# Kernel tuning notes

Hardware: AMD Instinct MI355X
Metric: run time of the kernel (lower is better)

## Reference

```python
import jax, jax.numpy as jnp
import numpy as np


def setup_inputs() -> dict:
    key = jax.random.key(0)
    ks = jax.random.split(key, 7)
    B, N, D, A = 32, 128, 512, 512
    sD = 1.0 / np.sqrt(D)
    sA = 1.0 / np.sqrt(A)
    return {
        "x": jax.random.normal(ks[0], (B, N, D), dtype=jnp.float32),
        "W1": jax.random.normal(ks[1], (A, D), dtype=jnp.float32) * sD,
        "b1": jax.random.normal(ks[2], (A,), dtype=jnp.float32) * sD,
        "W2": jax.random.normal(ks[3], (A, D), dtype=jnp.float32) * sD,
        "b2": jax.random.normal(ks[4], (A,), dtype=jnp.float32) * sD,
        "Wout": jax.random.normal(ks[5], (A,), dtype=jnp.float32) * sA,
        "bout": jax.random.normal(ks[6], (1,), dtype=jnp.float32) * sA,
    }


def reference(x, W1, b1, W2, b2, Wout, bout):
    # x: (B, N, D)
    x1 = jnp.einsum('bnd,ad->bna', x, W1) + b1  # mlp1 -> (B, N, A)
    x2 = jnp.einsum('bnd,ad->bna', x, W2) + b2  # mlp2 -> (B, N, A)
    # outer broadcast add: x1.unsqueeze(1) + x2.unsqueeze(2) -> (B, N, N, A)
    s = x1[:, None, :, :] + x2[:, :, None, :]
    # include_root=False: drop ROOT row along dim 1 -> (B, N-1, N, A)
    s = s[:, 1:, :, :]
    s = jnp.tanh(s)
    # out linear A -> 1, then squeeze -> (B, N-1, N)
    return jnp.einsum('bija,a->bij', s, Wout) + bout[0]
```

## Files before the change

kernel.cpp:

```cpp
#include <hip/hip_runtime.h>
#include <hip/hip_bf16.h>

#define B_ 32
#define N_ 128
#define D_ 512
#define A_ 512
#define R_ (B_*N_)
#define OC (2*A_)
#define CEXP 2.8853900817779268f

typedef __attribute__((ext_vector_type(8))) short  frag_ab;
typedef __attribute__((ext_vector_type(4))) float  frag_cd;

__device__ inline unsigned pack2bf(float a, float b) {
    unsigned ua = __builtin_bit_cast(unsigned, a) + 0x8000u;
    unsigned ub = __builtin_bit_cast(unsigned, b) + 0x8000u;
    return __builtin_amdgcn_perm(ub, ua, 0x07060302);
}

__global__ __launch_bounds__(256) void k1_mfma(
    const float* __restrict__ X,
    const float* __restrict__ W1, const float* __restrict__ b1,
    const float* __restrict__ W2, const float* __restrict__ b2,
    float* __restrict__ Y)
{
    __shared__ unsigned short As[128*32];
    __shared__ unsigned short Bs[128*32];

    const int t    = threadIdx.x;
    const int lane = t & 63;
    const int wid  = t >> 6;
    const int wr   = wid >> 1;
    const int wc   = wid & 1;
    const int row0 = blockIdx.x * 128;
    const int col0 = blockIdx.y * 128;
    const float* Wb = (col0 < A_) ? W1 : W2;
    const float* bb = (col0 < A_) ? b1 : b2;
    const int wrow0 = col0 & (A_-1);

    const int srow = t >> 2;
    const int sk8  = (t & 3) * 8;

    frag_cd acc[4][4];
#pragma unroll
    for (int i = 0; i < 4; ++i)
#pragma unroll
        for (int j = 0; j < 4; ++j) acc[i][j] = frag_cd{0.f,0.f,0.f,0.f};

    const int fr = lane & 15;
    const int ko = (lane >> 4) * 8;

    for (int k0 = 0; k0 < D_; k0 += 32) {
        float4 xv[2][2], wv[2][2];
#pragma unroll
        for (int q = 0; q < 2; ++q) {
            const int row = q*64 + srow;
            const float* px = &X [(size_t)(row0  + row) * D_ + k0 + sk8];
            const float* pw = &Wb[(size_t)(wrow0 + row) * D_ + k0 + sk8];
            xv[q][0] = *(const float4*)px;  xv[q][1] = *(const float4*)(px+4);
            wv[q][0] = *(const float4*)pw;  wv[q][1] = *(const float4*)(pw+4);
        }
        __syncthreads();
#pragma unroll
        for (int q = 0; q < 2; ++q) {
            const int row = q*64 + srow;
            uint4 pa, pb;
            pa.x = pack2bf(xv[q][0].x, xv[q][0].y);
            pa.y = pack2bf(xv[q][0].z, xv[q][0].w);
            pa.z = pack2bf(xv[q][1].x, xv[q][1].y);
            pa.w = pack2bf(xv[q][1].z, xv[q][1].w);
            pb.x = pack2bf(wv[q][0].x, wv[q][0].y);
            pb.y = pack2bf(wv[q][0].z, wv[q][0].w);
            pb.z = pack2bf(wv[q][1].x, wv[q][1].y);
            pb.w = pack2bf(wv[q][1].z, wv[q][1].w);
            *reinterpret_cast<uint4*>(&As[row*32 + sk8]) = pa;
            *reinterpret_cast<uint4*>(&Bs[row*32 + sk8]) = pb;
        }
        __syncthreads();
        frag_ab af[4], bfv[4];
#pragma unroll
        for (int fi = 0; fi < 4; ++fi)
            af[fi]  = *reinterpret_cast<const frag_ab*>(&As[(wr*64 + fi*16 + fr)*32 + ko]);
#pragma unroll
        for (int fj = 0; fj < 4; ++fj)
            bfv[fj] = *reinterpret_cast<const frag_ab*>(&Bs[(wc*64 + fj*16 + fr)*32 + ko]);
#pragma unroll
        for (int fi = 0; fi < 4; ++fi)
#pragma unroll
            for (int fj = 0; fj < 4; ++fj)
                acc[fi][fj] = __builtin_amdgcn_mfma_f32_16x16x32_bf16(
                    af[fi], bfv[fj], acc[fi][fj], 0, 0, 0);
    }

#pragma unroll
    for (int fi = 0; fi < 4; ++fi) {
        const int rr = row0 + wr*64 + fi*16 + (lane >> 4)*4;
#pragma unroll
        for (int fj = 0; fj < 4; ++fj) {
            const int cc = col0 + wc*64 + fj*16 + (lane & 15);
            const float bias = bb[cc & (A_-1)];
#pragma unroll
            for (int r = 0; r < 4; ++r)
                Y[(size_t)(rr + r) * OC + cc] =
                    __builtin_amdgcn_exp2f(CEXP * (acc[fi][fj][r] + bias));
        }
    }
}

#define ACH 128

__global__ __launch_bounds__(256) void k2_tanh(
    const float* __restrict__ Y,
    const float* __restrict__ Wout,
    const float* __restrict__ bout,
    float* __restrict__ out)
{
    __shared__ float e1s[32][ACH + 4];
    __shared__ float e2s[32][ACH + 4];
    __shared__ float wo[A_];
    __shared__ float wsum_s[4];

    const int t  = threadIdx.x;
    const int jt = blockIdx.x;
    const int it = blockIdx.y;
    const int b  = blockIdx.z;

    float ws = 0.f;
    for (int k = t; k < A_; k += 256) { float w = Wout[k]; wo[k] = w; ws += w; }
#pragma unroll
    for (int off = 32; off >= 1; off >>= 1) ws += __shfl_down(ws, off, 64);
    if ((t & 63) == 0) wsum_s[t >> 6] = ws;

    const float* yb = Y + (size_t)b * N_ * OC;
    const int sr = t >> 5;
    const int sc = (t & 31) * 4;

    float4 c1[4], c2[4], n1[4], n2[4];
#pragma unroll
    for (int q = 0; q < 4; ++q) {
        const int r = q*8 + sr;
        c1[q] = *(const float4*)&yb[(size_t)(jt*32 + r) * OC + sc];
        int i2 = it*32 + r + 1; if (i2 > 127) i2 = 127;
        c2[q] = *(const float4*)&yb[(size_t)i2 * OC + A_ + sc];
    }

    const int jl = t & 15;
    const int il = t >> 4;
    float a00 = 0.f, a01 = 0.f, a10 = 0.f, a11 = 0.f;

    for (int a0 = 0; a0 < A_; a0 += ACH) {
        __syncthreads();
#pragma unroll
        for (int q = 0; q < 4; ++q) {
            const int r = q*8 + sr;
            *(float4*)&e1s[r][sc] = c1[q];
            *(float4*)&e2s[r][sc] = c2[q];
        }
        __syncthreads();
        if (a0 + ACH < A_) {
#pragma unroll
            for (int q = 0; q < 4; ++q) {
                const int r = q*8 + sr;
                n1[q] = *(const float4*)&yb[(size_t)(jt*32 + r) * OC + (a0 + ACH) + sc];
                int i2 = it*32 + r + 1; if (i2 > 127) i2 = 127;
                n2[q] = *(const float4*)&yb[(size_t)i2 * OC + A_ + (a0 + ACH) + sc];
            }
        }
#pragma unroll 4
        for (int c = 0; c < ACH; c += 4) {
            float4 u0 = *(const float4*)&e1s[jl     ][c];
            float4 u1 = *(const float4*)&e1s[jl + 16][c];
            float4 v0 = *(const float4*)&e2s[il     ][c];
            float4 v1 = *(const float4*)&e2s[il + 16][c];
            float4 w  = *(const float4*)&wo[a0 + c];
            a00 += w.x * __builtin_amdgcn_rcpf(fmaf(u0.x, v0.x, 1.f));
            a01 += w.x * __builtin_amdgcn_rcpf(fmaf(u1.x, v0.x, 1.f));
            a10 += w.x * __builtin_amdgcn_rcpf(fmaf(u0.x, v1.x, 1.f));
            a11 += w.x * __builtin_amdgcn_rcpf(fmaf(u1.x, v1.x, 1.f));
            a00 += w.y * __builtin_amdgcn_rcpf(fmaf(u0.y, v0.y, 1.f));
            a01 += w.y * __builtin_amdgcn_rcpf(fmaf(u1.y, v0.y, 1.f));
            a10 += w.y * __builtin_amdgcn_rcpf(fmaf(u0.y, v1.y, 1.f));
            a11 += w.y * __builtin_amdgcn_rcpf(fmaf(u1.y, v1.y, 1.f));
            a00 += w.z * __builtin_amdgcn_rcpf(fmaf(u0.z, v0.z, 1.f));
            a01 += w.z * __builtin_amdgcn_rcpf(fmaf(u1.z, v0.z, 1.f));
            a10 += w.z * __builtin_amdgcn_rcpf(fmaf(u0.z, v1.z, 1.f));
            a11 += w.z * __builtin_amdgcn_rcpf(fmaf(u1.z, v1.z, 1.f));
            a00 += w.w * __builtin_amdgcn_rcpf(fmaf(u0.w, v0.w, 1.f));
            a01 += w.w * __builtin_amdgcn_rcpf(fmaf(u1.w, v0.w, 1.f));
            a10 += w.w * __builtin_amdgcn_rcpf(fmaf(u0.w, v1.w, 1.f));
            a11 += w.w * __builtin_amdgcn_rcpf(fmaf(u1.w, v1.w, 1.f));
        }
#pragma unroll
        for (int q = 0; q < 4; ++q) { c1[q] = n1[q]; c2[q] = n2[q]; }
    }

    const float wsum = wsum_s[0] + wsum_s[1] + wsum_s[2] + wsum_s[3];
    const float bo   = bout[0];
    const int i0 = it*32 + il;
    const int j0 = jt*32 + jl;

    if (i0 < 127)      out[((size_t)(b*127) + i0     ) * 128 + j0     ] = wsum - 2.f*a00 + bo;
    if (i0 < 127)      out[((size_t)(b*127) + i0     ) * 128 + j0 + 16] = wsum - 2.f*a01 + bo;
    if (i0 + 16 < 127) out[((size_t)(b*127) + i0 + 16) * 128 + j0     ] = wsum - 2.f*a10 + bo;
    if (i0 + 16 < 127) out[((size_t)(b*127) + i0 + 16) * 128 + j0 + 16] = wsum - 2.f*a11 + bo;
}

extern "C" void kernel_launch(void* const* d_in, const int* in_sizes, int n_in,
                              void* d_out, int out_size, void* d_ws, size_t ws_size,
                              hipStream_t stream) {
    const float* x    = (const float*)d_in[0];
    const float* W1   = (const float*)d_in[1];
    const float* b1   = (const float*)d_in[2];
    const float* W2   = (const float*)d_in[3];
    const float* b2   = (const float*)d_in[4];
    const float* Wout = (const float*)d_in[5];
    const float* bout = (const float*)d_in[6];
    float* out = (float*)d_out;
    float* Y   = (float*)d_ws;

    dim3 g1(R_/128, OC/128);
    k1_mfma<<<g1, 256, 0, stream>>>(x, W1, b1, W2, b2, Y);

    dim3 g2(4, 4, B_);
    k2_tanh<<<g2, 256, 0, stream>>>(Y, Wout, bout, out);
}
```

Before: 130.4 us.

## Pre-convert GEMM inputs to bf16, double-buffer LDS, store intermediates as bf16

Adds a conversion kernel that turns X, W1 and W2 into bf16 before the GEMM. The GEMM now loads bf16 directly, uses a BK=64 double-buffered LDS pipeline with padded rows, and writes its exp outputs as bf16. The tanh kernel reads bf16 intermediates, converts them to float in LDS, and double-buffers its chunks. This halves intermediate memory traffic and removes per-tile conversion work from the GEMM. In exchange it adds an extra kernel launch plus a pass over X, and loses precision in the stored exp values.

```diff
diff --git a/kernel.cpp b/kernel.cpp
--- a/kernel.cpp
+++ b/kernel.cpp
@@ -6,7 +6,7 @@
 #define D_ 512
 #define A_ 512
 #define R_ (B_*N_)
-#define OC (2*A_)
+#define OC 1024
 #define CEXP 2.8853900817779268f
 
 typedef __attribute__((ext_vector_type(8))) short  frag_ab;
@@ -17,161 +17,204 @@
     unsigned ub = __builtin_bit_cast(unsigned, b) + 0x8000u;
     return __builtin_amdgcn_perm(ub, ua, 0x07060302);
 }
+__device__ inline float bf2f_lo(unsigned u){ return __builtin_bit_cast(float, u << 16); }
+__device__ inline float bf2f_hi(unsigned u){ return __builtin_bit_cast(float, u & 0xffff0000u); }
+
+__global__ __launch_bounds__(256) void k0_cvt(
+    const float* __restrict__ X, const float* __restrict__ W1,
+    const float* __restrict__ W2,
+    unsigned short* __restrict__ Xb, unsigned short* __restrict__ W1b,
+    unsigned short* __restrict__ W2b)
+{
+    const int NX = R_*D_/8, NW = A_*D_/8;
+    int i = blockIdx.x*256 + threadIdx.x;
+    const float* src; unsigned short* dst; int off;
+    if (i < NX)            { src = X;  dst = Xb;  off = i; }
+    else if (i < NX+NW)    { src = W1; dst = W1b; off = i-NX; }
+    else if (i < NX+2*NW)  { src = W2; dst = W2b; off = i-NX-NW; }
+    else return;
+    float4 a = ((const float4*)src)[off*2];
+    float4 c = ((const float4*)src)[off*2+1];
+    uint4 o;
+    o.x = pack2bf(a.x,a.y); o.y = pack2bf(a.z,a.w);
+    o.z = pack2bf(c.x,c.y); o.w = pack2bf(c.z,c.w);
+    ((uint4*)dst)[off] = o;
+}
+
+#define BK1 64
+#define LDK 68
 
 __global__ __launch_bounds__(256) void k1_mfma(
-    const float* __restrict__ X,
-    const float* __restrict__ W1, const float* __restrict__ b1,
-    const float* __restrict__ W2, const float* __restrict__ b2,
-    float* __restrict__ Y)
+    const unsigned short* __restrict__ Xb,
+    const unsigned short* __restrict__ W1b, const float* __restrict__ b1,
+    const unsigned short* __restrict__ W2b, const float* __restrict__ b2,
+    unsigned short* __restrict__ Yb)
 {
-    __shared__ unsigned short As[128*32];
-    __shared__ unsigned short Bs[128*32];
-
-    const int t    = threadIdx.x;
-    const int lane = t & 63;
-    const int wid  = t >> 6;
-    const int wr   = wid >> 1;
-    const int wc   = wid & 1;
-    const int row0 = blockIdx.x * 128;
-    const int col0 = blockIdx.y * 128;
-    const float* Wb = (col0 < A_) ? W1 : W2;
+    __shared__ unsigned short As[2][128*LDK];
+    __shared__ unsigned short Bs[2][128*LDK];
+
+    const int t = threadIdx.x, lane = t&63, wid = t>>6;
+    const int wr = wid>>1, wc = wid&1;
+    const int row0 = blockIdx.x*128, col0 = blockIdx.y*128;
+    const unsigned short* Wb = (col0 < A_) ? W1b : W2b;
     const float* bb = (col0 < A_) ? b1 : b2;
     const int wrow0 = col0 & (A_-1);
 
-    const int srow = t >> 2;
-    const int sk8  = (t & 3) * 8;
+    const int srow = t>>3;
+    const int scol = (t&7)*8;
 
     frag_cd acc[4][4];
 #pragma unroll
-    for (int i = 0; i < 4; ++i)
-#pragma unroll
-        for (int j = 0; j < 4; ++j) acc[i][j] = frag_cd{0.f,0.f,0.f,0.f};
-
-    const int fr = lane & 15;
-    const int ko = (lane >> 4) * 8;
-
-    for (int k0 = 0; k0 < D_; k0 += 32) {
-        float4 xv[2][2], wv[2][2];
-#pragma unroll
-        for (int q = 0; q < 2; ++q) {
-            const int row = q*64 + srow;
-            const float* px = &X [(size_t)(row0  + row) * D_ + k0 + sk8];
-            const float* pw = &Wb[(size_t)(wrow0 + row) * D_ + k0 + sk8];
-            xv[q][0] = *(const float4*)px;  xv[q][1] = *(const float4*)(px+4);
-            wv[q][0] = *(const float4*)pw;  wv[q][1] = *(const float4*)(pw+4);
+    for (int i=0;i<4;++i)
+#pragma unroll
+        for (int j=0;j<4;++j) acc[i][j] = frag_cd{0.f,0.f,0.f,0.f};
+
+    const int fr = lane&15, g8 = (lane>>4)*8;
+
+    uint4 ra[4], rb[4];
+#pragma unroll
+    for (int q=0;q<4;++q){
+        int r = q*32 + srow;
+        ra[q] = *(const uint4*)&Xb[(size_t)(row0 +r)*D_ + scol];
+        rb[q] = *(const uint4*)&Wb[(size_t)(wrow0+r)*D_ + scol];
+    }
+#pragma unroll
+    for (int q=0;q<4;++q){
+        int r = q*32 + srow;
+        *(uint4*)&As[0][r*LDK + scol] = ra[q];
+        *(uint4*)&Bs[0][r*LDK + scol] = rb[q];
+    }
+    __syncthreads();
+
+#pragma unroll
+    for (int s=0; s<8; ++s) {
+        const int cur = s&1;
+        if (s<7) {
+            const int k0 = (s+1)*BK1;
+#pragma unroll
+            for (int q=0;q<4;++q){
+                int r = q*32 + srow;
+                ra[q] = *(const uint4*)&Xb[(size_t)(row0 +r)*D_ + k0 + scol];
+                rb[q] = *(const uint4*)&Wb[(size_t)(wrow0+r)*D_ + k0 + scol];
+            }
+        }
+        frag_ab af[4][2], bf[4][2];
+#pragma unroll
+        for (int fi=0;fi<4;++fi)
+#pragma unroll
+            for (int ks=0;ks<2;++ks) {
+                af[fi][ks] = *(const frag_ab*)&As[cur][(wr*64+fi*16+fr)*LDK + ks*32 + g8];
+                bf[fi][ks] = *(const frag_ab*)&Bs[cur][(wc*64+fi*16+fr)*LDK + ks*32 + g8];
+            }
+#pragma unroll
+        for (int ks=0;ks<2;++ks)
+#pragma unroll
+            for (int fi=0;fi<4;++fi)
+#pragma unroll
+                for (int fj=0;fj<4;++fj)
+                    acc[fi][fj] = __builtin_amdgcn_mfma_f32_16x16x32_bf16(
+                        af[fi][ks], bf[fj][ks], acc[fi][fj], 0, 0, 0);
+        if (s<7) {
+#pragma unroll
+            for (int q=0;q<4;++q){
+                int r = q*32 + srow;
+                *(uint4*)&As[cur^1][r*LDK + scol] = ra[q];
+                *(uint4*)&Bs[cur^1][r*LDK + scol] = rb[q];
+            }
         }
         __syncthreads();
-#pragma unroll
-        for (int q = 0; q < 2; ++q) {
-            const int row = q*64 + srow;
-            uint4 pa, pb;
-            pa.x = pack2bf(xv[q][0].x, xv[q][0].y);
-            pa.y = pack2bf(xv[q][0].z, xv[q][0].w);
-            pa.z = pack2bf(xv[q][1].x, xv[q][1].y);
-            pa.w = pack2bf(xv[q][1].z, xv[q][1].w);
-            pb.x = pack2bf(wv[q][0].x, wv[q][0].y);
-            pb.y = pack2bf(wv[q][0].z, wv[q][0].w);
-            pb.z = pack2bf(wv[q][1].x, wv[q][1].y);
-            pb.w = pack2bf(wv[q][1].z, wv[q][1].w);
-            *reinterpret_cast<uint4*>(&As[row*32 + sk8]) = pa;
-            *reinterpret_cast<uint4*>(&Bs[row*32 + sk8]) = pb;
-        }
-        __syncthreads();
-        frag_ab af[4], bfv[4];
-#pragma unroll
-        for (int fi = 0; fi < 4; ++fi)
-            af[fi]  = *reinterpret_cast<const frag_ab*>(&As[(wr*64 + fi*16 + fr)*32 + ko]);
-#pragma unroll
-        for (int fj = 0; fj < 4; ++fj)
-            bfv[fj] = *reinterpret_cast<const frag_ab*>(&Bs[(wc*64 + fj*16 + fr)*32 + ko]);
-#pragma unroll
-        for (int fi = 0; fi < 4; ++fi)
-#pragma unroll
-            for (int fj = 0; fj < 4; ++fj)
-                acc[fi][fj] = __builtin_amdgcn_mfma_f32_16x16x32_bf16(
-                    af[fi], bfv[fj], acc[fi][fj], 0, 0, 0);
-    }
-
-#pragma unroll
-    for (int fi = 0; fi < 4; ++fi) {
-        const int rr = row0 + wr*64 + fi*16 + (lane >> 4)*4;
-#pragma unroll
-        for (int fj = 0; fj < 4; ++fj) {
-            const int cc = col0 + wc*64 + fj*16 + (lane & 15);
+    }
+
+#pragma unroll
+    for (int fi=0;fi<4;++fi){
+        const int rr = row0 + wr*64 + fi*16 + (lane>>4)*4;
+#pragma unroll
+        for (int fj=0;fj<4;++fj){
+            const int cc = col0 + wc*64 + fj*16 + (lane&15);
             const float bias = bb[cc & (A_-1)];
 #pragma unroll
-            for (int r = 0; r < 4; ++r)
-                Y[(size_t)(rr + r) * OC + cc] =
-                    __builtin_amdgcn_exp2f(CEXP * (acc[fi][fj][r] + bias));
+            for (int r=0;r<4;++r){
+                float e = __builtin_amdgcn_exp2f(CEXP*(acc[fi][fj][r] + bias));
+                Yb[(size_t)(rr+r)*OC + cc] =
+                    (unsigned short)((__builtin_bit_cast(unsigned, e) + 0x8000u) >> 16);
+            }
         }
     }
 }
 
 #define ACH 128
+#define LDA2 (ACH+4)
 
 __global__ __launch_bounds__(256) void k2_tanh(
-    const float* __restrict__ Y,
-    const float* __restrict__ Wout,
-    const float* __restrict__ bout,
+    const unsigned short* __restrict__ Yb,
+    const float* __restrict__ Wout, const float* __restrict__ bout,
     float* __restrict__ out)
 {
-    __shared__ float e1s[32][ACH + 4];
-    __shared__ float e2s[32][ACH + 4];
+    __shared__ float e1s[2][32][LDA2];
+    __shared__ float e2s[2][32][LDA2];
     __shared__ float wo[A_];
     __shared__ float wsum_s[4];
 
     const int t  = threadIdx.x;
-    const int jt = blockIdx.x;
-    const int it = blockIdx.y;
-    const int b  = blockIdx.z;
-
-    float ws = 0.f;
-    for (int k = t; k < A_; k += 256) { float w = Wout[k]; wo[k] = w; ws += w; }
-#pragma unroll
-    for (int off = 32; off >= 1; off >>= 1) ws += __shfl_down(ws, off, 64);
-    if ((t & 63) == 0) wsum_s[t >> 6] = ws;
-
-    const float* yb = Y + (size_t)b * N_ * OC;
-    const int sr = t >> 5;
-    const int sc = (t & 31) * 4;
-
-    float4 c1[4], c2[4], n1[4], n2[4];
-#pragma unroll
-    for (int q = 0; q < 4; ++q) {
-        const int r = q*8 + sr;
-        c1[q] = *(const float4*)&yb[(size_t)(jt*32 + r) * OC + sc];
-        int i2 = it*32 + r + 1; if (i2 > 127) i2 = 127;
-        c2[q] = *(const float4*)&yb[(size_t)i2 * OC + A_ + sc];
-    }
-
-    const int jl = t & 15;
-    const int il = t >> 4;
-    float a00 = 0.f, a01 = 0.f, a10 = 0.f, a11 = 0.f;
-
-    for (int a0 = 0; a0 < A_; a0 += ACH) {
-        __syncthreads();
-#pragma unroll
-        for (int q = 0; q < 4; ++q) {
-            const int r = q*8 + sr;
-            *(float4*)&e1s[r][sc] = c1[q];
-            *(float4*)&e2s[r][sc] = c2[q];
-        }
-        __syncthreads();
-        if (a0 + ACH < A_) {
-#pragma unroll
-            for (int q = 0; q < 4; ++q) {
-                const int r = q*8 + sr;
-                n1[q] = *(const float4*)&yb[(size_t)(jt*32 + r) * OC + (a0 + ACH) + sc];
-                int i2 = it*32 + r + 1; if (i2 > 127) i2 = 127;
-                n2[q] = *(const float4*)&yb[(size_t)i2 * OC + A_ + (a0 + ACH) + sc];
-            }
-        }
+    const int jt = blockIdx.x, it = blockIdx.y, b = blockIdx.z;
+
+    float wsacc = 0.f;
+    for (int k=t; k<A_; k+=256){ float w = Wout[k]; wo[k] = w; wsacc += w; }
+#pragma unroll
+    for (int off=32; off>=1; off>>=1) wsacc += __shfl_down(wsacc, off, 64);
+    if ((t&63)==0) wsum_s[t>>6] = wsacc;
+
+    const unsigned short* yb = Yb + (size_t)b*N_*OC;
+    const int sr = t>>4;
+    const int sc = (t&15)*8;
+
+    uint4 r1[2], r2[2];
+#pragma unroll
+    for (int q=0;q<2;++q){
+        int row = q*16 + sr;
+        r1[q] = *(const uint4*)&yb[(size_t)(jt*32+row)*OC + sc];
+        int i2 = it*32 + row + 1; if (i2 > 127) i2 = 127;
+        r2[q] = *(const uint4*)&yb[(size_t)i2*OC + A_ + sc];
+    }
+#pragma unroll
+    for (int q=0;q<2;++q){
+        int row = q*16 + sr;
+        uint4 v = r1[q];
+        float4 lo = {bf2f_lo(v.x), bf2f_hi(v.x), bf2f_lo(v.y), bf2f_hi(v.y)};
+        float4 hi = {bf2f_lo(v.z), bf2f_hi(v.z), bf2f_lo(v.w), bf2f_hi(v.w)};
+        *(float4*)&e1s[0][row][sc]   = lo;
+        *(float4*)&e1s[0][row][sc+4] = hi;
+        v = r2[q];
+        float4 lo2 = {bf2f_lo(v.x), bf2f_hi(v.x), bf2f_lo(v.y), bf2f_hi(v.y)};
+        float4 hi2 = {bf2f_lo(v.z), bf2f_hi(v.z), bf2f_lo(v.w), bf2f_hi(v.w)};
+        *(float4*)&e2s[0][row][sc]   = lo2;
+        *(float4*)&e2s[0][row][sc+4] = hi2;
+    }
+    __syncthreads();
+
+    const int jl = t&15, il = t>>4;
+    float a00=0.f, a01=0.f, a10=0.f, a11=0.f;
+
+#pragma unroll
+    for (int ch=0; ch<4; ++ch) {
+        const int cur = ch&1;
+        if (ch<3) {
+            const int a0n = (ch+1)*ACH;
+#pragma unroll
+            for (int q=0;q<2;++q){
+                int row = q*16 + sr;
+                r1[q] = *(const uint4*)&yb[(size_t)(jt*32+row)*OC + a0n + sc];
+                int i2 = it*32 + row + 1; if (i2 > 127) i2 = 127;
+                r2[q] = *(const uint4*)&yb[(size_t)i2*OC + A_ + a0n + sc];
+            }
+        }
+        const int a0 = ch*ACH;
 #pragma unroll 4
-        for (int c = 0; c < ACH; c += 4) {
-            float4 u0 = *(const float4*)&e1s[jl     ][c];
-            float4 u1 = *(const float4*)&e1s[jl + 16][c];
-            float4 v0 = *(const float4*)&e2s[il     ][c];
-            float4 v1 = *(const float4*)&e2s[il + 16][c];
+        for (int c=0; c<ACH; c+=4) {
+            float4 u0 = *(const float4*)&e1s[cur][jl     ][c];
+            float4 u1 = *(const float4*)&e1s[cur][jl + 16][c];
+            float4 v0 = *(const float4*)&e2s[cur][il     ][c];
+            float4 v1 = *(const float4*)&e2s[cur][il + 16][c];
             float4 w  = *(const float4*)&wo[a0 + c];
             a00 += w.x * __builtin_amdgcn_rcpf(fmaf(u0.x, v0.x, 1.f));
             a01 += w.x * __builtin_amdgcn_rcpf(fmaf(u1.x, v0.x, 1.f));
@@ -190,8 +233,23 @@
             a10 += w.w * __builtin_amdgcn_rcpf(fmaf(u0.w, v1.w, 1.f));
             a11 += w.w * __builtin_amdgcn_rcpf(fmaf(u1.w, v1.w, 1.f));
         }
-#pragma unroll
-        for (int q = 0; q < 4; ++q) { c1[q] = n1[q]; c2[q] = n2[q]; }
+        if (ch<3) {
+#pragma unroll
+            for (int q=0;q<2;++q){
+                int row = q*16 + sr;
+                uint4 v = r1[q];
+                float4 lo = {bf2f_lo(v.x), bf2f_hi(v.x), bf2f_lo(v.y), bf2f_hi(v.y)};
+                float4 hi = {bf2f_lo(v.z), bf2f_hi(v.z), bf2f_lo(v.w), bf2f_hi(v.w)};
+                *(float4*)&e1s[cur^1][row][sc]   = lo;
+                *(float4*)&e1s[cur^1][row][sc+4] = hi;
+                v = r2[q];
+                float4 lo2 = {bf2f_lo(v.x), bf2f_hi(v.x), bf2f_lo(v.y), bf2f_hi(v.y)};
+                float4 hi2 = {bf2f_lo(v.z), bf2f_hi(v.z), bf2f_lo(v.w), bf2f_hi(v.w)};
+                *(float4*)&e2s[cur^1][row][sc]   = lo2;
+                *(float4*)&e2s[cur^1][row][sc+4] = hi2;
+            }
+            __syncthreads();
+        }
     }
 
     const float wsum = wsum_s[0] + wsum_s[1] + wsum_s[2] + wsum_s[3];
@@ -216,11 +274,18 @@
     const float* Wout = (const float*)d_in[5];
     const float* bout = (const float*)d_in[6];
     float* out = (float*)d_out;
-    float* Y   = (float*)d_ws;
+
+    char* ws = (char*)d_ws;
+    unsigned short* Yb  = (unsigned short*)ws;
+    unsigned short* Xb  = (unsigned short*)(ws + (8u<<20));
+    unsigned short* W1b = (unsigned short*)(ws + (12u<<20));
+    unsigned short* W2b = (unsigned short*)(ws + (12u<<20) + (1u<<19));
+
+    k0_cvt<<<1280, 256, 0, stream>>>(x, W1, W2, Xb, W1b, W2b);
 
     dim3 g1(R_/128, OC/128);
-    k1_mfma<<<g1, 256, 0, stream>>>(x, W1, b1, W2, b2, Y);
+    k1_mfma<<<g1, 256, 0, stream>>>(Xb, W1b, b1, W2b, b2, Yb);
 
     dim3 g2(4, 4, B_);
-    k2_tanh<<<g2, 256, 0, stream>>>(Y, Wout, bout, out);
-}
+    k2_tanh<<<g2, 256, 0, stream>>>(Yb, Wout, bout, out);
+}
```

New measurement: 131.1 us. About the same (+0.5%).
